# Performance work log

Measured on AMD Instinct MI355X. Metric: run time of the kernel, lower is better.

The kernel has to match this reference:

```python
import jax, jax.numpy as jnp
import numpy as np

VOCAB = 100000; D = 300; F_NUM = 768
M = 64; N = 16
SURF_L = 4; CTX_L = 50; DOC_L = 100; BODY_L = 200
HEADS = 5


def _conv_relu_avg(x, W, b):
    # x: [B, L, D] tokens-embedded; conv1d (valid) + relu + global avgpool -> [B, F]
    y = jax.lax.conv_general_dilated(x.transpose(0, 2, 1), W, (1,), 'VALID',
                                     dimension_numbers=('NCH', 'OIH', 'NCH'))
    return jax.nn.relu(y + b[None, :, None]).mean(axis=2)


def _mha(q, k, v, num_heads=HEADS):
    # split-head scaled dot-product attention (no learned projections), q:[Lq,D] k,v:[Lk,D]
    Lq, Dm = q.shape
    hd = Dm // num_heads
    qh = q.reshape(Lq, num_heads, hd).transpose(1, 0, 2)
    kh = k.reshape(k.shape[0], num_heads, hd).transpose(1, 0, 2)
    vh = v.reshape(v.shape[0], num_heads, hd).transpose(1, 0, 2)
    att = jax.nn.softmax(jnp.einsum('hqd,hkd->hqk', qh, kh) * (1.0 / np.sqrt(hd)), axis=-1)
    out = jnp.einsum('hqk,hkd->hqd', att, vh)
    return out.transpose(1, 0, 2).reshape(Lq, Dm)


def _cos(a, b, eps=1e-6):
    na = jnp.maximum(jnp.sqrt((a * a).sum(-1)), eps)
    nb = jnp.maximum(jnp.sqrt((b * b).sum(-1)), eps)
    return (a * b).sum(-1) / (na * nb)


def setup_inputs() -> dict:
    key = jax.random.key(0)
    ks = jax.random.split(key, 20)
    inp = {}
    inp['mention_entity'] = jnp.ones((M, N), dtype=jnp.int32)
    inp['m'] = M
    inp['n'] = N
    inp['mention_vec'] = jax.random.randint(ks[0], (M, SURF_L), 0, VOCAB)
    inp['context_vec'] = jax.random.randint(ks[1], (M, CTX_L), 0, VOCAB)
    inp['doc_vec'] = jax.random.randint(ks[2], (DOC_L,), 0, VOCAB)
    inp['title_vec'] = jax.random.normal(ks[3], (N, F_NUM), dtype=jnp.float32)
    inp['body_vec'] = jax.random.randint(ks[4], (N, BODY_L), 0, VOCAB)
    inp['sfeats'] = jnp.zeros((N, 1), dtype=jnp.float32)
    inp['m2c_prior'] = jax.random.uniform(ks[5], (N,), dtype=jnp.float32)
    inp['men2cands'] = jax.random.randint(ks[6], (M, N), 0, VOCAB)
    inp['contexts_ids'] = jax.random.randint(ks[7], (M, CTX_L), 0, VOCAB)
    inp['hand_features'] = jax.random.uniform(ks[8], (N, 1), dtype=jnp.float32)
    inp['bert_doc_vec'] = jax.random.normal(ks[9], (1, F_NUM), dtype=jnp.float32)
    # learned parameters
    inp['embed_table'] = jax.random.normal(ks[10], (VOCAB, D), dtype=jnp.float32) * 0.1
    inp['conv_ms_w'] = jax.random.normal(ks[11], (F_NUM, D, 2), dtype=jnp.float32) * 0.05
    inp['conv_ms_b'] = jnp.zeros((F_NUM,), dtype=jnp.float32)
    inp['conv_mc_w'] = jax.random.normal(ks[12], (F_NUM, D, 5), dtype=jnp.float32) * 0.05
    inp['conv_mc_b'] = jnp.zeros((F_NUM,), dtype=jnp.float32)
    inp['layer_local_w'] = jax.random.normal(ks[13], (7,), dtype=jnp.float32) * 0.3
    inp['layer_local_b'] = jnp.zeros((), dtype=jnp.float32)
    inp['att_w1'] = jax.random.normal(ks[14], (600, 300), dtype=jnp.float32) * 0.05
    inp['att_b1'] = jnp.zeros((300,), dtype=jnp.float32)
    inp['att_w2'] = jax.random.normal(ks[15], (300, 1), dtype=jnp.float32) * 0.05
    inp['att_b2'] = jnp.zeros((), dtype=jnp.float32)
    return inp


def reference(mention_entity, m, n, mention_vec, context_vec, doc_vec, title_vec,
              body_vec, sfeats, m2c_prior, men2cands, contexts_ids, hand_features,
              bert_doc_vec, embed_table, conv_ms_w, conv_ms_b, conv_mc_w, conv_mc_b,
              layer_local_w, layer_local_b, att_w1, att_b1, att_w2, att_b2):
    # per-mention conv features (vectorized over all mentions at once)
    ms = _conv_relu_avg(embed_table[mention_vec], conv_ms_w, conv_ms_b)   # [M,768]
    mc = _conv_relu_avg(embed_table[context_vec], conv_mc_w, conv_mc_b)   # [M,768]
    md = bert_doc_vec[0]                                                  # [768]
    doc_emb = embed_table[doc_vec]                                        # [100,300]
    body_emb = embed_table[body_vec]                                      # [N,200,300]

    # per-candidate cross attention doc<->body, max-pooled over query positions
    att_d_b = jax.vmap(lambda b: _mha(doc_emb, b, b).max(axis=0))(body_emb)          # [N,300]
    att_b_d = jax.vmap(lambda b: _mha(b, doc_emb, doc_emb).max(axis=0))(body_emb)    # [N,300]
    comb = jnp.concatenate([att_d_b, att_b_d], axis=-1)                              # [N,600]
    att_score = jax.nn.sigmoid(jax.nn.relu(comb @ att_w1 + att_b1) @ att_w2 + att_b2)[:, 0]  # [N]

    # LocalCtxAttRanker: candidate-vs-context attention score
    ctx_emb = embed_table[contexts_ids]                                   # [M,50,300]
    cand_emb = embed_table[men2cands]                                     # [M,N,300]
    tok = jnp.einsum('mnd,mtd->mnt', cand_emb, ctx_emb)                   # [M,N,50]
    p = jax.nn.softmax(tok.max(axis=1), axis=-1)                          # [M,50]
    ctxv = jnp.einsum('mt,mtd->md', p, ctx_emb)                           # [M,300]
    local_att = jnp.einsum('mnd,md->mn', cand_emb, ctxv)                  # [M,N]

    cos_st = _cos(ms[:, None, :], title_vec[None, :, :])                  # [M,N]
    cos_dt = _cos(md[None, :], title_vec)                                 # [N]
    cos_ct = _cos(mc[:, None, :], title_vec[None, :, :])                  # [M,N]

    Mm = ms.shape[0]
    bc = lambda v: jnp.broadcast_to(v[None, :], (Mm, v.shape[0]))
    # feature order matches torch.cat((hand_fea, prior, localAtt, attScore, C_score))
    feats = jnp.stack([bc(hand_features[:, 0]), bc(m2c_prior), local_att,
                       bc(att_score), cos_st, bc(cos_dt), cos_ct], axis=-1)  # [M,N,7]
    score = feats @ layer_local_w + layer_local_b                         # [M,N]

    # per-mention standardization (unbiased std, as torch.std), softmax and uniform renorm
    mu = score.mean(axis=1, keepdims=True)
    sd = score.std(axis=1, keepdims=True, ddof=1)
    z = (score - mu) / sd
    sm = jax.nn.softmax(z, axis=1)
    zmin = z.min(axis=1, keepdims=True)
    zmax = z.max(axis=1, keepdims=True)
    u = (z + 1.0 - zmin) / (zmax - zmin)
    u = u / u.sum(axis=1, keepdims=True)
    return (z, sm, u)
```

## Files before the change

### kernel.cpp

```cpp
#include <hip/hip_runtime.h>

#define MM 64
#define NN 16
#define DDIM 300
#define FNUM 768
#define SURF_LL 4
#define CTX_LL 50
#define DOC_LL 100
#define BODY_LL 200
#define NHEADS 5
#define HDIM 60

#define GM 2944
#define GK 1536
#define GN 768

typedef unsigned short u16;
typedef unsigned int u32;
typedef __attribute__((ext_vector_type(8))) short short8;
typedef __attribute__((ext_vector_type(4))) float f32x4;

#define OFF_MSG    0
#define OFF_CTX2G  76800
#define OFF_CANDG  1036800
#define OFF_MS     1344000
#define OFF_MC     1393152
#define OFF_PV0    1442304
#define OFF_PV1    1451904
#define OFF_ASC    1471104
#define OFF_LATT   1471120
#define OFF_ABF    1472144
#define OFF_WTMC   (OFF_ABF + GM*GK/2)
#define OFF_WTMS   (OFF_WTMC + GN*GK/2)
#define OFF_P      (OFF_WTMS + 600*768)

__device__ __forceinline__ u16 f2bf(float x) {
  union { float f; u32 u; } v; v.f = x;
  u32 r = v.u + 0x7FFFu + ((v.u >> 16) & 1u);
  return (u16)(r >> 16);
}

__global__ __launch_bounds__(256) void mega_prep_kernel(
    const float* __restrict__ embed,
    const int* __restrict__ mention_vec,
    const int* __restrict__ context_vec,
    const int* __restrict__ contexts_ids,
    const int* __restrict__ men2cands,
    const float* __restrict__ Wmc,
    const float* __restrict__ Wms,
    float* __restrict__ dst, float* __restrict__ mc,
    u32* __restrict__ Abf, u32* __restrict__ WTmc, float* __restrict__ WTms) {
  int bid = blockIdx.x;
  if (bid < 5250) {
    int e = bid * 256 + threadIdx.x;
    int row = e / DDIM;
    int col = e - row * DDIM;
    int tok;
    if (row < 256)       tok = mention_vec[row];
    else if (row < 3456) tok = contexts_ids[row - 256];
    else                 tok = men2cands[row - 3456];
    dst[e] = embed[(size_t)tok * DDIM + col];
  } else if (bid < 5442) {
    mc[(bid - 5250) * 256 + threadIdx.x] = 0.f;
  } else if (bid < 14274) {
    int idx = (bid - 5442) * 256 + threadIdx.x;
    int r = idx / (GK / 2);
    int kp = idx - r * (GK / 2);
    int k = kp * 2;
    int m = r / 46, t = r - m * 46;
    u32 out = 0;
#pragma unroll
    for (int j = 0; j < 2; j++) {
      int kj = k + j;
      u16 h = 0;
      if (kj < 1500) {
        int tap = kj / 300;
        int d = kj - tap * 300;
        int tok = context_vec[m * CTX_LL + t + tap];
        h = f2bf(embed[(size_t)tok * DDIM + d]);
      }
      out |= (u32)h << (16 * j);
    }
    Abf[idx] = out;
  } else if (bid < 16578) {
    int idx = (bid - 14274) * 256 + threadIdx.x;
    int n = idx / (GK / 2);
    int kp = idx - n * (GK / 2);
    int k = kp * 2;
    u32 out = 0;
#pragma unroll
    for (int j = 0; j < 2; j++) {
      int kj = k + j;
      u16 h = 0;
      if (kj < 1500) {
        int tap = kj / 300;
        int d = kj - tap * 300;
        h = f2bf(Wmc[(size_t)n * 1500 + d * 5 + tap]);
      }
      out |= (u32)h << (16 * j);
    }
    WTmc[idx] = out;
  } else {
    int idx = (bid - 16578) * 256 + threadIdx.x;
    int k = idx / FNUM;
    int f = idx - k * FNUM;
    WTms[idx] = Wms[(size_t)f * 600 + k];
  }
}

__global__ __launch_bounds__(256) void conv_gemm_kernel(
    const u16* __restrict__ A,
    const u16* __restrict__ B,
    const float* __restrict__ bias,
    float* __restrict__ mc) {
  int bn = blockIdx.x, bm = blockIdx.y;
  __shared__ u16 As[64][72];
  __shared__ u16 Bs[64][72];
  int tid = threadIdx.x;
  int w = tid >> 6, lane = tid & 63;
  int wr = w >> 1, wc = w & 1;
  int lg = lane >> 4, lm = lane & 15;
  f32x4 acc[2][2];
#pragma unroll
  for (int i = 0; i < 2; i++)
#pragma unroll
    for (int j = 0; j < 2; j++) acc[i][j] = (f32x4)0.f;
  int c0row = tid >> 3, ck = (tid & 7) * 8;
  const u16* Ag = A + (size_t)(bm * 64) * GK;
  const u16* Bg = B + (size_t)(bn * 64) * GK;
  for (int kt = 0; kt < GK / 64; kt++) {
    int k0 = kt * 64;
    uint4 av0 = *(const uint4*)(Ag + (size_t)c0row * GK + k0 + ck);
    uint4 av1 = *(const uint4*)(Ag + (size_t)(c0row + 32) * GK + k0 + ck);
    uint4 bv0 = *(const uint4*)(Bg + (size_t)c0row * GK + k0 + ck);
    uint4 bv1 = *(const uint4*)(Bg + (size_t)(c0row + 32) * GK + k0 + ck);
    __syncthreads();
    *(uint4*)&As[c0row][ck] = av0;
    *(uint4*)&As[c0row + 32][ck] = av1;
    *(uint4*)&Bs[c0row][ck] = bv0;
    *(uint4*)&Bs[c0row + 32][ck] = bv1;
    __syncthreads();
#pragma unroll
    for (int kk = 0; kk < 2; kk++) {
      short8 af0 = *(const short8*)&As[wr * 32 + lm][kk * 32 + lg * 8];
      short8 af1 = *(const short8*)&As[wr * 32 + 16 + lm][kk * 32 + lg * 8];
      short8 bf0 = *(const short8*)&Bs[wc * 32 + lm][kk * 32 + lg * 8];
      short8 bf1 = *(const short8*)&Bs[wc * 32 + 16 + lm][kk * 32 + lg * 8];
      acc[0][0] = __builtin_amdgcn_mfma_f32_16x16x32_bf16(af0, bf0, acc[0][0], 0, 0, 0);
      acc[0][1] = __builtin_amdgcn_mfma_f32_16x16x32_bf16(af0, bf1, acc[0][1], 0, 0, 0);
      acc[1][0] = __builtin_amdgcn_mfma_f32_16x16x32_bf16(af1, bf0, acc[1][0], 0, 0, 0);
      acc[1][1] = __builtin_amdgcn_mfma_f32_16x16x32_bf16(af1, bf1, acc[1][1], 0, 0, 0);
    }
  }
#pragma unroll
  for (int mf = 0; mf < 2; mf++)
#pragma unroll
    for (int nf = 0; nf < 2; nf++) {
      int col = bn * 64 + wc * 32 + nf * 16 + lm;
      float bb = bias[col];
      int base = bm * 64 + wr * 32 + mf * 16 + lg * 4;
      int mcur = base / 46;
      float s = 0.f;
#pragma unroll
      for (int r = 0; r < 4; r++) {
        float v = fmaxf(acc[mf][nf][r] + bb, 0.f) * (1.0f / 46.0f);
        int mm = (base + r) / 46;
        if (mm != mcur) { atomicAdd(&mc[mcur * FNUM + col], s); s = 0.f; mcur = mm; }
        s += v;
      }
      atomicAdd(&mc[mcur * FNUM + col], s);
    }
}

__device__ __forceinline__ void conv_ms_body(
    const float* __restrict__ msg, const float* __restrict__ WT,
    const float* __restrict__ B, float* __restrict__ ms, int b) {
  int m = b / 3, fi = b - m * 3;
  int f = fi * 256 + threadIdx.x;
  const float* x = msg + m * SURF_LL * DDIM;
  float a0 = 0.f, a1 = 0.f, a2 = 0.f;
  for (int d = 0; d < DDIM; d++) {
    float v0 = x[d], v1 = x[DDIM + d], v2 = x[2 * DDIM + d], v3 = x[3 * DDIM + d];
    float wA = WT[(size_t)(2 * d) * FNUM + f];
    float wB = WT[(size_t)(2 * d + 1) * FNUM + f];
    a0 += v0 * wA + v1 * wB;
    a1 += v1 * wA + v2 * wB;
    a2 += v2 * wA + v3 * wB;
  }
  float bb = B[f];
  float r = fmaxf(a0 + bb, 0.f) + fmaxf(a1 + bb, 0.f) + fmaxf(a2 + bb, 0.f);
  ms[m * FNUM + f] = r * (1.0f / 3.0f);
}

template <int DIR>
__device__ __forceinline__ void scores_body(
    const float* __restrict__ embed, const int* __restrict__ doc_vec,
    const int* __restrict__ body_vec, float* __restrict__ P, int b,
    float* __restrict__ smem) {
  constexpr int Lq = DIR ? 200 : 100;
  constexpr int Lk = DIR ? 100 : 200;
  constexpr int KPL = DIR ? 2 : 4;
  int qt = b / 80;
  int rem = b - qt * 80;
  int n = rem / 5, h = rem - n * 5;
  const int* qids = DIR ? body_vec + n * BODY_LL : doc_vec;
  const int* kids = DIR ? doc_vec : body_vec + n * BODY_LL;
  float* Ks = smem;
  float* Qs = smem + Lk * 62;
  for (int idx = threadIdx.x; idx < Lk * 15; idx += 256) {
    int r = idx / 15, c = idx - r * 15;
    float4 v = *(const float4*)(embed + (size_t)kids[r] * DDIM + h * HDIM + c * 4);
    float* dp = Ks + r * 62 + c * 4;
    dp[0] = v.x; dp[1] = v.y; dp[2] = v.z; dp[3] = v.w;
  }
  for (int idx = threadIdx.x; idx < 32 * 15; idx += 256) {
    int r = idx / 15, c = idx - r * 15;
    int q = qt * 32 + r; if (q >= Lq) q = Lq - 1;
    float4 v = *(const float4*)(embed + (size_t)qids[q] * DDIM + h * HDIM + c * 4);
    float* dp = Qs + r * 64 + c * 4;
    dp[0] = v.x; dp[1] = v.y; dp[2] = v.z; dp[3] = v.w;
  }
  __syncthreads();
  int w = threadIdx.x >> 6, lane = threadIdx.x & 63;
  int kcl[KPL];
#pragma unroll
  for (int j = 0; j < KPL; j++) {
    int kk = lane + 64 * j; kcl[j] = (kk < Lk) ? kk : (Lk - 1);
  }
  float acc[8][KPL];
#pragma unroll
  for (int i = 0; i < 8; i++)
#pragma unroll
    for (int j = 0; j < KPL; j++) acc[i][j] = 0.f;
  for (int d = 0; d < HDIM; d += 4) {
    float2 kva[KPL], kvb[KPL];
#pragma unroll
    for (int j = 0; j < KPL; j++) {
      kva[j] = *(const float2*)&Ks[kcl[j] * 62 + d];
      kvb[j] = *(const float2*)&Ks[kcl[j] * 62 + d + 2];
    }
#pragma unroll
    for (int i = 0; i < 8; i++) {
      float4 qv = *(const float4*)&Qs[(w * 8 + i) * 64 + d];
#pragma unroll
      for (int j = 0; j < KPL; j++)
        acc[i][j] += qv.x * kva[j].x + qv.y * kva[j].y +
                     qv.z * kvb[j].x + qv.w * kvb[j].y;
    }
  }
  const float scale = 0.12909944487358056f;
#pragma unroll
  for (int i = 0; i < 8; i++) {
    int q = qt * 32 + w * 8 + i;
    float mx = -1e30f;
#pragma unroll
    for (int j = 0; j < KPL; j++)
      if (lane + 64 * j < Lk) mx = fmaxf(mx, acc[i][j]);
#pragma unroll
    for (int o = 32; o >= 1; o >>= 1) mx = fmaxf(mx, __shfl_xor(mx, o));
    float mxs = mx * scale;
    float p[KPL];
    float s = 0.f;
#pragma unroll
    for (int j = 0; j < KPL; j++) {
      p[j] = (lane + 64 * j < Lk) ? __expf(acc[i][j] * scale - mxs) : 0.f;
      s += p[j];
    }
#pragma unroll
    for (int o = 32; o >= 1; o >>= 1) s += __shfl_xor(s, o);
    float inv = 1.0f / s;
    if (q < Lq) {
      float* rowp = P + (size_t)((n * 2 + DIR) * NHEADS + h) * 20000 + q * Lk;
#pragma unroll
      for (int j = 0; j < KPL; j++) {
        int kk = lane + 64 * j;
        if (kk < Lk) rowp[kk] = p[j] * inv;
      }
    }
  }
}

__device__ __forceinline__ void tokctxv_body(
    const float* __restrict__ candg, const float* __restrict__ ctx2g,
    float* __restrict__ local_att, int m, float* __restrict__ smem) {
  float* cand  = smem;
  float* ctx   = smem + 4800;
  float* tokb  = smem + 9600;
  float* tkmx  = smem + 9872;
  float* pp    = smem + 9936;
  float* sctxv = smem + 10000;
  int tid = threadIdx.x;
  for (int i = tid; i < NN * DDIM; i += 256)
    cand[i] = candg[(size_t)m * NN * DDIM + i];
  int nI = tid >> 4, tt = tid & 15;
  for (int tile = 0; tile < 4; tile++) {
    int cbase = tile * 16;
    __syncthreads();
    for (int i = tid; i < 16 * DDIM; i += 256) {
      int rr = i / DDIM, cc = i - rr * DDIM;
      int t = cbase + rr;
      ctx[rr * DDIM + cc] = (t < CTX_LL) ? ctx2g[(size_t)(m * CTX_LL + t) * DDIM + cc] : 0.f;
    }
    __syncthreads();
    const float4* ca = (const float4*)(cand + nI * DDIM);
    const float4* cb = (const float4*)(ctx + tt * DDIM);
    float dsum = 0.f;
#pragma unroll
    for (int c = 0; c < 75; c++) {
      float4 a = ca[c], b = cb[c];
      dsum += a.x * b.x + a.y * b.y + a.z * b.z + a.w * b.w;
    }
    tokb[nI * 17 + tt] = dsum;
    __syncthreads();
    if (tid < 16) {
      float mx = -1e30f;
      for (int nn = 0; nn < NN; nn++) mx = fmaxf(mx, tokb[nn * 17 + tid]);
      int t = cbase + tid;
      if (t < CTX_LL) tkmx[t] = mx;
    }
  }
  __syncthreads();
  if (tid < 64) {
    float v = (tid < CTX_LL) ? tkmx[tid] : -1e30f;
    float mx = v;
#pragma unroll
    for (int o = 32; o >= 1; o >>= 1) mx = fmaxf(mx, __shfl_xor(mx, o));
    float e = (tid < CTX_LL) ? expf(v - mx) : 0.f;
    float s = e;
#pragma unroll
    for (int o = 32; o >= 1; o >>= 1) s += __shfl_xor(s, o);
    pp[tid] = e / s;
  }
  __syncthreads();
  for (int d = tid; d < DDIM; d += 256) {
    float acc = 0.f;
    for (int t = 0; t < CTX_LL; t++)
      acc += pp[t] * ctx2g[(size_t)(m * CTX_LL + t) * DDIM + d];
    sctxv[d] = acc;
  }
  __syncthreads();
  int j = tid & 15;
  float dd = 0.f;
  for (int i = j; i < DDIM; i += 16) dd += cand[nI * DDIM + i] * sctxv[i];
#pragma unroll
  for (int o = 8; o >= 1; o >>= 1) dd += __shfl_xor(dd, o);
  if (j == 0) local_att[m * NN + nI] = dd;
}

__global__ __launch_bounds__(256) void mega_mid_kernel(
    const float* __restrict__ embed,
    const int* __restrict__ doc_vec,
    const int* __restrict__ body_vec,
    const float* __restrict__ msg,
    const float* __restrict__ WTms,
    const float* __restrict__ Bms,
    const float* __restrict__ candg,
    const float* __restrict__ ctx2g,
    float* __restrict__ ms,
    float* __restrict__ P,
    float* __restrict__ local_att) {
  __shared__ float smem[14448];
  int bid = blockIdx.x;
  if (bid < 192) {
    conv_ms_body(msg, WTms, Bms, ms, bid);
  } else if (bid < 512) {
    scores_body<0>(embed, doc_vec, body_vec, P, bid - 192, smem);
  } else if (bid < 1072) {
    scores_body<1>(embed, doc_vec, body_vec, P, bid - 512, smem);
  } else {
    tokctxv_body(candg, ctx2g, local_att, bid - 1072, smem);
  }
}

__global__ __launch_bounds__(256) void attn_pv_kernel(
    const float* __restrict__ embed,
    const int* __restrict__ doc_vec,
    const int* __restrict__ body_vec,
    const float* __restrict__ P,
    float* __restrict__ pv0,
    float* __restrict__ pv1) {
  int bid = blockIdx.x;
  int dir, pt, n, h;
  if (bid < 160) { dir = 0; h = bid % 5; n = (bid / 5) % 16; pt = bid / 80; }
  else { int b = bid - 160; dir = 1; h = b % 5; n = (b / 5) % 16; pt = b / 80; }
  int Lq = dir ? 200 : 100;
  int Lk = dir ? 100 : 200;
  int Lk4 = Lk >> 2;
  int K4STR = dir ? 27 : 51;
  const int* kids = dir ? doc_vec : body_vec + n * BODY_LL;
  __shared__ float4 Kt4[60 * 51];
  __shared__ float red[4][64];
  float* Ktf = (float*)Kt4;
  int RS = K4STR * 4;
  for (int idx = threadIdx.x; idx < Lk * 15; idx += 256) {
    int r = idx / 15, c = idx - r * 15;
    float4 v = *(const float4*)(embed + (size_t)kids[r] * DDIM + h * HDIM + c * 4);
    Ktf[(c * 4 + 0) * RS + r] = v.x;
    Ktf[(c * 4 + 1) * RS + r] = v.y;
    Ktf[(c * 4 + 2) * RS + r] = v.z;
    Ktf[(c * 4 + 3) * RS + r] = v.w;
  }
  __syncthreads();
  int lane = threadIdx.x & 63;
  int w = __builtin_amdgcn_readfirstlane(threadIdx.x >> 6);
  int dl = (lane < HDIM) ? lane : (HDIM - 1);
  const float4* Krow = Kt4 + dl * K4STR;
  const float* Pb = P + (size_t)((n * 2 + dir) * NHEADS + h) * 20000;
  float omax = -1e30f;
#pragma unroll
  for (int p = 0; p < 4; p++) {
    int q0 = pt * 64 + p * 16 + w * 4;
    int qa0 = min(q0, Lq - 1), qa1 = min(q0 + 1, Lq - 1);
    int qa2 = min(q0 + 2, Lq - 1), qa3 = min(q0 + 3, Lq - 1);
    const float4* P0 = (const float4*)(Pb + (size_t)qa0 * Lk);
    const float4* P1 = (const float4*)(Pb + (size_t)qa1 * Lk);
    const float4* P2 = (const float4*)(Pb + (size_t)qa2 * Lk);
    const float4* P3 = (const float4*)(Pb + (size_t)qa3 * Lk);
    float o0 = 0.f, o1 = 0.f, o2 = 0.f, o3 = 0.f;
    for (int k4 = 0; k4 < Lk4; k4++) {
      float4 pp0 = P0[k4], pp1 = P1[k4], pp2 = P2[k4], pp3 = P3[k4];
      float4 kk = Krow[k4];
      o0 += pp0.x * kk.x + pp0.y * kk.y + pp0.z * kk.z + pp0.w * kk.w;
      o1 += pp1.x * kk.x + pp1.y * kk.y + pp1.z * kk.z + pp1.w * kk.w;
      o2 += pp2.x * kk.x + pp2.y * kk.y + pp2.z * kk.z + pp2.w * kk.w;
      o3 += pp3.x * kk.x + pp3.y * kk.y + pp3.z * kk.z + pp3.w * kk.w;
    }
    if (q0 < Lq)     omax = fmaxf(omax, o0);
    if (q0 + 1 < Lq) omax = fmaxf(omax, o1);
    if (q0 + 2 < Lq) omax = fmaxf(omax, o2);
    if (q0 + 3 < Lq) omax = fmaxf(omax, o3);
  }
  red[threadIdx.x >> 6][lane] = omax;
  __syncthreads();
  if (threadIdx.x < 64 && lane < HDIM) {
    float m4 = fmaxf(fmaxf(red[0][lane], red[1][lane]),
                     fmaxf(red[2][lane], red[3][lane]));
    float* dst = dir ? pv1 + (size_t)((n * NHEADS + h) * 4 + pt) * HDIM
                     : pv0 + (size_t)((n * NHEADS + h) * 2 + pt) * HDIM;
    dst[lane] = m4;
  }
}

__global__ __launch_bounds__(256) void mlp_kernel(
    const float* __restrict__ pv0, const float* __restrict__ pv1,
    const float* __restrict__ w1, const float* __restrict__ b1,
    const float* __restrict__ w2, const float* __restrict__ b2,
    float* __restrict__ att_score) {
  int n = blockIdx.x, tid = threadIdx.x;
  __shared__ float comb[600];
  for (int idx = tid; idx < 300; idx += 256) {
    int h = idx / 60, d = idx - h * 60;
    float mx = -1e30f;
#pragma unroll
    for (int pt = 0; pt < 2; pt++)
      mx = fmaxf(mx, pv0[(size_t)((n * NHEADS + h) * 2 + pt) * HDIM + d]);
    comb[idx] = mx;
    mx = -1e30f;
#pragma unroll
    for (int pt = 0; pt < 4; pt++)
      mx = fmaxf(mx, pv1[(size_t)((n * NHEADS + h) * 4 + pt) * HDIM + d]);
    comb[300 + idx] = mx;
  }
  __syncthreads();
  float partial = 0.f;
  for (int j = tid; j < 300; j += 256) {
    float hh = b1[j];
    for (int k = 0; k < 600; k++) hh += comb[k] * w1[k * 300 + j];
    partial += fmaxf(hh, 0.f) * w2[j];
  }
  __shared__ float redd[256];
  redd[tid] = partial;
  __syncthreads();
  for (int s = 128; s > 0; s >>= 1) {
    if (tid < s) redd[tid] += redd[tid + s];
    __syncthreads();
  }
  if (tid == 0) att_score[n] = 1.0f / (1.0f + expf(-(redd[0] + b2[0])));
}

__global__ __launch_bounds__(256) void final_kernel(
    const float* __restrict__ ms,
    const float* __restrict__ mc,
    const float* __restrict__ title,
    const float* __restrict__ bert,
    const float* __restrict__ att_score,
    const float* __restrict__ m2c_prior,
    const float* __restrict__ hand,
    const float* __restrict__ local_att,
    const float* __restrict__ w7,
    const float* __restrict__ b7,
    float* __restrict__ out) {
  int m = blockIdx.x, tid = threadIdx.x;
  __shared__ float sms[FNUM], smc[FNUM], smd[FNUM];
  __shared__ float snorm[3], sscore[16], wred[3][4];
  for (int i = tid; i < FNUM; i += 256) {
    sms[i] = ms[m * FNUM + i];
    smc[i] = mc[m * FNUM + i];
    smd[i] = bert[i];
  }
  __syncthreads();
  float p1 = 0.f, p2 = 0.f, p3 = 0.f;
  for (int i = tid; i < FNUM; i += 256) {
    float a = sms[i], b = smc[i], c = smd[i];
    p1 += a * a; p2 += b * b; p3 += c * c;
  }
#pragma unroll
  for (int o = 32; o >= 1; o >>= 1) {
    p1 += __shfl_xor(p1, o); p2 += __shfl_xor(p2, o); p3 += __shfl_xor(p3, o);
  }
  int wid = tid >> 6, lane = tid & 63;
  if (lane == 0) { wred[0][wid] = p1; wred[1][wid] = p2; wred[2][wid] = p3; }
  __syncthreads();
  if (tid == 0) {
    snorm[0] = fmaxf(sqrtf(wred[0][0] + wred[0][1] + wred[0][2] + wred[0][3]), 1e-6f);
    snorm[1] = fmaxf(sqrtf(wred[1][0] + wred[1][1] + wred[1][2] + wred[1][3]), 1e-6f);
    snorm[2] = fmaxf(sqrtf(wred[2][0] + wred[2][1] + wred[2][2] + wred[2][3]), 1e-6f);
  }
  __syncthreads();
  int nI = tid >> 4, j = tid & 15;
  float d1 = 0.f, d2 = 0.f, d3 = 0.f, d4 = 0.f;
  for (int i = j; i < FNUM; i += 16) {
    float t = title[nI * FNUM + i];
    d1 += sms[i] * t; d2 += smc[i] * t; d3 += smd[i] * t; d4 += t * t;
  }
#pragma unroll
  for (int o = 8; o >= 1; o >>= 1) {
    d1 += __shfl_xor(d1, o); d2 += __shfl_xor(d2, o);
    d3 += __shfl_xor(d3, o); d4 += __shfl_xor(d4, o);
  }
  if (j == 0) {
    float nt = fmaxf(sqrtf(d4), 1e-6f);
    float cos_st = d1 / (snorm[0] * nt);
    float cos_ct = d2 / (snorm[1] * nt);
    float cos_dt = d3 / (snorm[2] * nt);
    float score = hand[nI] * w7[0] + m2c_prior[nI] * w7[1] +
                  local_att[m * NN + nI] * w7[2] + att_score[nI] * w7[3] +
                  cos_st * w7[4] + cos_dt * w7[5] + cos_ct * w7[6] + b7[0];
    sscore[nI] = score;
  }
  __syncthreads();
  if (tid < 16) {
    float x = sscore[tid];
    float s = x;
#pragma unroll
    for (int o = 8; o >= 1; o >>= 1) s += __shfl_xor(s, o);
    float mu = s * (1.0f / 16.0f);
    float dv = (x - mu) * (x - mu);
    float vs = dv;
#pragma unroll
    for (int o = 8; o >= 1; o >>= 1) vs += __shfl_xor(vs, o);
    float sd = sqrtf(vs * (1.0f / 15.0f));
    float z = (x - mu) / sd;
    float zm = z;
#pragma unroll
    for (int o = 8; o >= 1; o >>= 1) zm = fmaxf(zm, __shfl_xor(zm, o));
    float e = expf(z - zm);
    float es = e;
#pragma unroll
    for (int o = 8; o >= 1; o >>= 1) es += __shfl_xor(es, o);
    float sm = e / es;
    float zmin = z;
#pragma unroll
    for (int o = 8; o >= 1; o >>= 1) zmin = fminf(zmin, __shfl_xor(zmin, o));
    float u0 = (z + 1.0f - zmin) / (zm - zmin);
    float us = u0;
#pragma unroll
    for (int o = 8; o >= 1; o >>= 1) us += __shfl_xor(us, o);
    float u = u0 / us;
    out[m * NN + tid] = z;
    out[MM * NN + m * NN + tid] = sm;
    out[2 * MM * NN + m * NN + tid] = u;
  }
}

extern "C" void kernel_launch(void* const* d_in, const int* in_sizes, int n_in,
                              void* d_out, int out_size, void* d_ws, size_t ws_size,
                              hipStream_t stream) {
  const int*   mention_vec   = (const int*)d_in[3];
  const int*   context_vec   = (const int*)d_in[4];
  const int*   doc_vec       = (const int*)d_in[5];
  const float* title_vec     = (const float*)d_in[6];
  const int*   body_vec      = (const int*)d_in[7];
  const float* m2c_prior     = (const float*)d_in[9];
  const int*   men2cands     = (const int*)d_in[10];
  const int*   contexts_ids  = (const int*)d_in[11];
  const float* hand_features = (const float*)d_in[12];
  const float* bert_doc_vec  = (const float*)d_in[13];
  const float* embed_table   = (const float*)d_in[14];
  const float* conv_ms_w     = (const float*)d_in[15];
  const float* conv_ms_b     = (const float*)d_in[16];
  const float* conv_mc_w     = (const float*)d_in[17];
  const float* conv_mc_b     = (const float*)d_in[18];
  const float* layer_local_w = (const float*)d_in[19];
  const float* layer_local_b = (const float*)d_in[20];
  const float* att_w1        = (const float*)d_in[21];
  const float* att_b1        = (const float*)d_in[22];
  const float* att_w2        = (const float*)d_in[23];
  const float* att_b2        = (const float*)d_in[24];

  float* ws     = (float*)d_ws;
  float* msg    = ws + OFF_MSG;
  float* ctx2g  = ws + OFF_CTX2G;
  float* candg  = ws + OFF_CANDG;
  float* ms     = ws + OFF_MS;
  float* mc     = ws + OFF_MC;
  float* pv0    = ws + OFF_PV0;
  float* pv1    = ws + OFF_PV1;
  float* att_sc = ws + OFF_ASC;
  float* latt   = ws + OFF_LATT;
  u16*   Abf    = (u16*)(ws + OFF_ABF);
  u16*   WTmc   = (u16*)(ws + OFF_WTMC);
  float* WTms   = ws + OFF_WTMS;
  float* P      = ws + OFF_P;
  float* out    = (float*)d_out;

  mega_prep_kernel<<<dim3(18378), dim3(256), 0, stream>>>(
      embed_table, mention_vec, context_vec, contexts_ids, men2cands,
      conv_mc_w, conv_ms_w, ws, mc, (u32*)Abf, (u32*)WTmc, WTms);
  conv_gemm_kernel<<<dim3(GN / 64, GM / 64), dim3(256), 0, stream>>>(
      Abf, WTmc, conv_mc_b, mc);
  mega_mid_kernel<<<dim3(1136), dim3(256), 0, stream>>>(
      embed_table, doc_vec, body_vec, msg, WTms, conv_ms_b, candg, ctx2g,
      ms, P, latt);
  attn_pv_kernel<<<dim3(480), dim3(256), 0, stream>>>(
      embed_table, doc_vec, body_vec, P, pv0, pv1);
  mlp_kernel<<<dim3(NN), dim3(256), 0, stream>>>(pv0, pv1, att_w1, att_b1, att_w2, att_b2, att_sc);
  final_kernel<<<dim3(MM), dim3(256), 0, stream>>>(
      ms, mc, title_vec, bert_doc_vec, att_sc, m2c_prior, hand_features,
      latt, layer_local_w, layer_local_b, out);
}
```

Baseline: 420.1 us.

## Fuse attention PV into scores kernel and split MLP across more blocks

The attention probability matrix P is no longer written to global memory. Each scores block now keeps its softmax rows in registers and shared memory, computes P·V against the keys already staged in shared memory, and writes per-tile max-pooled partials, so the separate attn_pv kernel and its P round trip disappear. The MLP moves from 16 blocks to 80, each handling a slice of hidden units, and combines results with atomicAdd into a logit buffer that the prep kernel zeroes. The final sigmoid moves into final_kernel. In exchange, shared memory use and register pressure in the mid kernel rise, and float atomics make the summation order nondeterministic.

Result: faster. 399.1 us (-5.0%).

```diff
diff --git a/kernel.cpp b/kernel.cpp
--- a/kernel.cpp
+++ b/kernel.cpp
@@ -26,13 +26,12 @@
 #define OFF_MS     1344000
 #define OFF_MC     1393152
 #define OFF_PV0    1442304
-#define OFF_PV1    1451904
-#define OFF_ASC    1471104
-#define OFF_LATT   1471120
-#define OFF_ABF    1472144
+#define OFF_PV1    1461504
+#define OFF_ASC    1495104
+#define OFF_LATT   1495120
+#define OFF_ABF    1496144
 #define OFF_WTMC   (OFF_ABF + GM*GK/2)
 #define OFF_WTMS   (OFF_WTMC + GN*GK/2)
-#define OFF_P      (OFF_WTMS + 600*768)
 
 __device__ __forceinline__ u16 f2bf(float x) {
   union { float f; u32 u; } v; v.f = x;
@@ -49,6 +48,7 @@
     const float* __restrict__ Wmc,
     const float* __restrict__ Wms,
     float* __restrict__ dst, float* __restrict__ mc,
+    float* __restrict__ att_logit,
     u32* __restrict__ Abf, u32* __restrict__ WTmc, float* __restrict__ WTms) {
   int bid = blockIdx.x;
   if (bid < 5250) {
@@ -62,8 +62,10 @@
     dst[e] = embed[(size_t)tok * DDIM + col];
   } else if (bid < 5442) {
     mc[(bid - 5250) * 256 + threadIdx.x] = 0.f;
-  } else if (bid < 14274) {
-    int idx = (bid - 5442) * 256 + threadIdx.x;
+  } else if (bid == 5442) {
+    if (threadIdx.x < NN) att_logit[threadIdx.x] = 0.f;
+  } else if (bid < 14275) {
+    int idx = (bid - 5443) * 256 + threadIdx.x;
     int r = idx / (GK / 2);
     int kp = idx - r * (GK / 2);
     int k = kp * 2;
@@ -82,8 +84,8 @@
       out |= (u32)h << (16 * j);
     }
     Abf[idx] = out;
-  } else if (bid < 16578) {
-    int idx = (bid - 14274) * 256 + threadIdx.x;
+  } else if (bid < 16579) {
+    int idx = (bid - 14275) * 256 + threadIdx.x;
     int n = idx / (GK / 2);
     int kp = idx - n * (GK / 2);
     int k = kp * 2;
@@ -101,7 +103,7 @@
     }
     WTmc[idx] = out;
   } else {
-    int idx = (bid - 16578) * 256 + threadIdx.x;
+    int idx = (bid - 16579) * 256 + threadIdx.x;
     int k = idx / FNUM;
     int f = idx - k * FNUM;
     WTms[idx] = Wms[(size_t)f * 600 + k];
@@ -193,20 +195,24 @@
 }
 
 template <int DIR>
-__device__ __forceinline__ void scores_body(
+__device__ __forceinline__ void scores_pv_body(
     const float* __restrict__ embed, const int* __restrict__ doc_vec,
-    const int* __restrict__ body_vec, float* __restrict__ P, int b,
+    const int* __restrict__ body_vec, float* __restrict__ pvp, int b,
     float* __restrict__ smem) {
   constexpr int Lq = DIR ? 200 : 100;
   constexpr int Lk = DIR ? 100 : 200;
   constexpr int KPL = DIR ? 2 : 4;
+  constexpr int NQT = DIR ? 7 : 4;
+  constexpr int NHALF = DIR ? 1 : 2;
   int qt = b / 80;
   int rem = b - qt * 80;
   int n = rem / 5, h = rem - n * 5;
   const int* qids = DIR ? body_vec + n * BODY_LL : doc_vec;
   const int* kids = DIR ? doc_vec : body_vec + n * BODY_LL;
   float* Ks = smem;
-  float* Qs = smem + Lk * 62;
+  float* Qs = smem + 12400;
+  float* Pl = smem + 12400;
+  float* red = smem + 15600;
   for (int idx = threadIdx.x; idx < Lk * 15; idx += 256) {
     int r = idx / 15, c = idx - r * 15;
     float4 v = *(const float4*)(embed + (size_t)kids[r] * DDIM + h * HDIM + c * 4);
@@ -251,7 +257,6 @@
   const float scale = 0.12909944487358056f;
 #pragma unroll
   for (int i = 0; i < 8; i++) {
-    int q = qt * 32 + w * 8 + i;
     float mx = -1e30f;
 #pragma unroll
     for (int j = 0; j < KPL; j++)
@@ -269,14 +274,52 @@
 #pragma unroll
     for (int o = 32; o >= 1; o >>= 1) s += __shfl_xor(s, o);
     float inv = 1.0f / s;
-    if (q < Lq) {
-      float* rowp = P + (size_t)((n * 2 + DIR) * NHEADS + h) * 20000 + q * Lk;
-#pragma unroll
-      for (int j = 0; j < KPL; j++) {
-        int kk = lane + 64 * j;
-        if (kk < Lk) rowp[kk] = p[j] * inv;
+#pragma unroll
+    for (int j = 0; j < KPL; j++) acc[i][j] = p[j] * inv;
+  }
+  __syncthreads();
+  float o[8];
+#pragma unroll
+  for (int i = 0; i < 8; i++) o[i] = 0.f;
+  int dl = (lane < HDIM) ? lane : (HDIM - 1);
+#pragma unroll
+  for (int half = 0; half < NHALF; half++) {
+    int kbase = half * 100;
+#pragma unroll
+    for (int j = 0; j < KPL; j++) {
+      int kk = lane + 64 * j;
+      int rel = kk - kbase;
+      if (rel >= 0 && rel < 100 && kk < Lk) {
+#pragma unroll
+        for (int i = 0; i < 8; i++)
+          Pl[(w * 8 + i) * 100 + rel] = acc[i][j];
       }
     }
+    for (int k4 = 0; k4 < 25; k4++) {
+      int k = kbase + k4 * 4;
+      float kv0 = Ks[(k + 0) * 62 + dl];
+      float kv1 = Ks[(k + 1) * 62 + dl];
+      float kv2 = Ks[(k + 2) * 62 + dl];
+      float kv3 = Ks[(k + 3) * 62 + dl];
+#pragma unroll
+      for (int i = 0; i < 8; i++) {
+        float4 pq = *(const float4*)&Pl[(w * 8 + i) * 100 + k4 * 4];
+        o[i] += pq.x * kv0 + pq.y * kv1 + pq.z * kv2 + pq.w * kv3;
+      }
+    }
+  }
+  float omax = -1e30f;
+#pragma unroll
+  for (int i = 0; i < 8; i++) {
+    int q = qt * 32 + w * 8 + i;
+    if (q < Lq) omax = fmaxf(omax, o[i]);
+  }
+  red[w * 64 + lane] = omax;
+  __syncthreads();
+  if (threadIdx.x < 64 && lane < HDIM) {
+    float m4 = fmaxf(fmaxf(red[0 * 64 + lane], red[1 * 64 + lane]),
+                     fmaxf(red[2 * 64 + lane], red[3 * 64 + lane]));
+    pvp[((size_t)(n * NHEADS + h) * NQT + qt) * HDIM + lane] = m4;
   }
 }
 
@@ -357,125 +400,66 @@
     const float* __restrict__ candg,
     const float* __restrict__ ctx2g,
     float* __restrict__ ms,
-    float* __restrict__ P,
+    float* __restrict__ pv0,
+    float* __restrict__ pv1,
     float* __restrict__ local_att) {
-  __shared__ float smem[14448];
+  __shared__ float smem[15856];
   int bid = blockIdx.x;
   if (bid < 192) {
     conv_ms_body(msg, WTms, Bms, ms, bid);
   } else if (bid < 512) {
-    scores_body<0>(embed, doc_vec, body_vec, P, bid - 192, smem);
+    scores_pv_body<0>(embed, doc_vec, body_vec, pv0, bid - 192, smem);
   } else if (bid < 1072) {
-    scores_body<1>(embed, doc_vec, body_vec, P, bid - 512, smem);
+    scores_pv_body<1>(embed, doc_vec, body_vec, pv1, bid - 512, smem);
   } else {
     tokctxv_body(candg, ctx2g, local_att, bid - 1072, smem);
-  }
-}
-
-__global__ __launch_bounds__(256) void attn_pv_kernel(
-    const float* __restrict__ embed,
-    const int* __restrict__ doc_vec,
-    const int* __restrict__ body_vec,
-    const float* __restrict__ P,
-    float* __restrict__ pv0,
-    float* __restrict__ pv1) {
-  int bid = blockIdx.x;
-  int dir, pt, n, h;
-  if (bid < 160) { dir = 0; h = bid % 5; n = (bid / 5) % 16; pt = bid / 80; }
-  else { int b = bid - 160; dir = 1; h = b % 5; n = (b / 5) % 16; pt = b / 80; }
-  int Lq = dir ? 200 : 100;
-  int Lk = dir ? 100 : 200;
-  int Lk4 = Lk >> 2;
-  int K4STR = dir ? 27 : 51;
-  const int* kids = dir ? doc_vec : body_vec + n * BODY_LL;
-  __shared__ float4 Kt4[60 * 51];
-  __shared__ float red[4][64];
-  float* Ktf = (float*)Kt4;
-  int RS = K4STR * 4;
-  for (int idx = threadIdx.x; idx < Lk * 15; idx += 256) {
-    int r = idx / 15, c = idx - r * 15;
-    float4 v = *(const float4*)(embed + (size_t)kids[r] * DDIM + h * HDIM + c * 4);
-    Ktf[(c * 4 + 0) * RS + r] = v.x;
-    Ktf[(c * 4 + 1) * RS + r] = v.y;
-    Ktf[(c * 4 + 2) * RS + r] = v.z;
-    Ktf[(c * 4 + 3) * RS + r] = v.w;
-  }
-  __syncthreads();
-  int lane = threadIdx.x & 63;
-  int w = __builtin_amdgcn_readfirstlane(threadIdx.x >> 6);
-  int dl = (lane < HDIM) ? lane : (HDIM - 1);
-  const float4* Krow = Kt4 + dl * K4STR;
-  const float* Pb = P + (size_t)((n * 2 + dir) * NHEADS + h) * 20000;
-  float omax = -1e30f;
-#pragma unroll
-  for (int p = 0; p < 4; p++) {
-    int q0 = pt * 64 + p * 16 + w * 4;
-    int qa0 = min(q0, Lq - 1), qa1 = min(q0 + 1, Lq - 1);
-    int qa2 = min(q0 + 2, Lq - 1), qa3 = min(q0 + 3, Lq - 1);
-    const float4* P0 = (const float4*)(Pb + (size_t)qa0 * Lk);
-    const float4* P1 = (const float4*)(Pb + (size_t)qa1 * Lk);
-    const float4* P2 = (const float4*)(Pb + (size_t)qa2 * Lk);
-    const float4* P3 = (const float4*)(Pb + (size_t)qa3 * Lk);
-    float o0 = 0.f, o1 = 0.f, o2 = 0.f, o3 = 0.f;
-    for (int k4 = 0; k4 < Lk4; k4++) {
-      float4 pp0 = P0[k4], pp1 = P1[k4], pp2 = P2[k4], pp3 = P3[k4];
-      float4 kk = Krow[k4];
-      o0 += pp0.x * kk.x + pp0.y * kk.y + pp0.z * kk.z + pp0.w * kk.w;
-      o1 += pp1.x * kk.x + pp1.y * kk.y + pp1.z * kk.z + pp1.w * kk.w;
-      o2 += pp2.x * kk.x + pp2.y * kk.y + pp2.z * kk.z + pp2.w * kk.w;
-      o3 += pp3.x * kk.x + pp3.y * kk.y + pp3.z * kk.z + pp3.w * kk.w;
-    }
-    if (q0 < Lq)     omax = fmaxf(omax, o0);
-    if (q0 + 1 < Lq) omax = fmaxf(omax, o1);
-    if (q0 + 2 < Lq) omax = fmaxf(omax, o2);
-    if (q0 + 3 < Lq) omax = fmaxf(omax, o3);
-  }
-  red[threadIdx.x >> 6][lane] = omax;
-  __syncthreads();
-  if (threadIdx.x < 64 && lane < HDIM) {
-    float m4 = fmaxf(fmaxf(red[0][lane], red[1][lane]),
-                     fmaxf(red[2][lane], red[3][lane]));
-    float* dst = dir ? pv1 + (size_t)((n * NHEADS + h) * 4 + pt) * HDIM
-                     : pv0 + (size_t)((n * NHEADS + h) * 2 + pt) * HDIM;
-    dst[lane] = m4;
   }
 }
 
 __global__ __launch_bounds__(256) void mlp_kernel(
     const float* __restrict__ pv0, const float* __restrict__ pv1,
     const float* __restrict__ w1, const float* __restrict__ b1,
-    const float* __restrict__ w2, const float* __restrict__ b2,
-    float* __restrict__ att_score) {
-  int n = blockIdx.x, tid = threadIdx.x;
+    const float* __restrict__ w2,
+    float* __restrict__ att_logit) {
+  int bid = blockIdx.x;
+  int n = bid / 5, jc = bid - n * 5;
+  int tid = threadIdx.x;
   __shared__ float comb[600];
-  for (int idx = tid; idx < 300; idx += 256) {
-    int h = idx / 60, d = idx - h * 60;
+  __shared__ float partial[4][64];
+  for (int idx = tid; idx < 600; idx += 256) {
+    int side = idx >= 300;
+    int pos = idx - side * 300;
+    int h = pos / 60, d = pos - h * 60;
     float mx = -1e30f;
-#pragma unroll
-    for (int pt = 0; pt < 2; pt++)
-      mx = fmaxf(mx, pv0[(size_t)((n * NHEADS + h) * 2 + pt) * HDIM + d]);
+    if (!side) {
+#pragma unroll
+      for (int pt = 0; pt < 4; pt++)
+        mx = fmaxf(mx, pv0[(size_t)((n * NHEADS + h) * 4 + pt) * HDIM + d]);
+    } else {
+#pragma unroll
+      for (int pt = 0; pt < 7; pt++)
+        mx = fmaxf(mx, pv1[(size_t)((n * NHEADS + h) * 7 + pt) * HDIM + d]);
+    }
     comb[idx] = mx;
-    mx = -1e30f;
-#pragma unroll
-    for (int pt = 0; pt < 4; pt++)
-      mx = fmaxf(mx, pv1[(size_t)((n * NHEADS + h) * 4 + pt) * HDIM + d]);
-    comb[300 + idx] = mx;
-  }
-  __syncthreads();
-  float partial = 0.f;
-  for (int j = tid; j < 300; j += 256) {
-    float hh = b1[j];
-    for (int k = 0; k < 600; k++) hh += comb[k] * w1[k * 300 + j];
-    partial += fmaxf(hh, 0.f) * w2[j];
-  }
-  __shared__ float redd[256];
-  redd[tid] = partial;
-  __syncthreads();
-  for (int s = 128; s > 0; s >>= 1) {
-    if (tid < s) redd[tid] += redd[tid + s];
-    __syncthreads();
-  }
-  if (tid == 0) att_score[n] = 1.0f / (1.0f + expf(-(redd[0] + b2[0])));
+  }
+  __syncthreads();
+  int w = tid >> 6, lane = tid & 63;
+  int jl = (lane < 60) ? lane : 59;
+  int jg = jc * 60 + jl;
+  float acc = 0.f;
+  for (int k = w; k < 600; k += 4)
+    acc += comb[k] * w1[(size_t)k * 300 + jg];
+  partial[w][lane] = acc;
+  __syncthreads();
+  if (tid < 64) {
+    float hv = partial[0][lane] + partial[1][lane] +
+               partial[2][lane] + partial[3][lane];
+    float hj = fmaxf(hv + b1[jg], 0.f) * w2[jg];
+    if (lane >= 60) hj = 0.f;
+#pragma unroll
+    for (int o = 32; o >= 1; o >>= 1) hj += __shfl_xor(hj, o);
+    if (lane == 0) atomicAdd(&att_logit[n], hj);
+  }
 }
 
 __global__ __launch_bounds__(256) void final_kernel(
@@ -483,7 +467,8 @@
     const float* __restrict__ mc,
     const float* __restrict__ title,
     const float* __restrict__ bert,
-    const float* __restrict__ att_score,
+    const float* __restrict__ att_logit,
+    const float* __restrict__ b2,
     const float* __restrict__ m2c_prior,
     const float* __restrict__ hand,
     const float* __restrict__ local_att,
@@ -533,8 +518,9 @@
     float cos_st = d1 / (snorm[0] * nt);
     float cos_ct = d2 / (snorm[1] * nt);
     float cos_dt = d3 / (snorm[2] * nt);
+    float asc = 1.0f / (1.0f + expf(-(att_logit[nI] + b2[0])));
     float score = hand[nI] * w7[0] + m2c_prior[nI] * w7[1] +
-                  local_att[m * NN + nI] * w7[2] + att_score[nI] * w7[3] +
+                  local_att[m * NN + nI] * w7[2] + asc * w7[3] +
                   cos_st * w7[4] + cos_dt * w7[5] + cos_ct * w7[6] + b7[0];
     sscore[nI] = score;
   }
@@ -606,26 +592,24 @@
   float* mc     = ws + OFF_MC;
   float* pv0    = ws + OFF_PV0;
   float* pv1    = ws + OFF_PV1;
-  float* att_sc = ws + OFF_ASC;
+  float* att_lg = ws + OFF_ASC;
   float* latt   = ws + OFF_LATT;
   u16*   Abf    = (u16*)(ws + OFF_ABF);
   u16*   WTmc   = (u16*)(ws + OFF_WTMC);
   float* WTms   = ws + OFF_WTMS;
-  float* P      = ws + OFF_P;
   float* out    = (float*)d_out;
 
-  mega_prep_kernel<<<dim3(18378), dim3(256), 0, stream>>>(
+  mega_prep_kernel<<<dim3(18379), dim3(256), 0, stream>>>(
       embed_table, mention_vec, context_vec, contexts_ids, men2cands,
-      conv_mc_w, conv_ms_w, ws, mc, (u32*)Abf, (u32*)WTmc, WTms);
+      conv_mc_w, conv_ms_w, ws, mc, att_lg, (u32*)Abf, (u32*)WTmc, WTms);
   conv_gemm_kernel<<<dim3(GN / 64, GM / 64), dim3(256), 0, stream>>>(
       Abf, WTmc, conv_mc_b, mc);
   mega_mid_kernel<<<dim3(1136), dim3(256), 0, stream>>>(
       embed_table, doc_vec, body_vec, msg, WTms, conv_ms_b, candg, ctx2g,
-      ms, P, latt);
-  attn_pv_kernel<<<dim3(480), dim3(256), 0, stream>>>(
-      embed_table, doc_vec, body_vec, P, pv0, pv1);
-  mlp_kernel<<<dim3(NN), dim3(256), 0, stream>>>(pv0, pv1, att_w1, att_b1, att_w2, att_b2, att_sc);
+      ms, pv0, pv1, latt);
+  mlp_kernel<<<dim3(80), dim3(256), 0, stream>>>(
+      pv0, pv1, att_w1, att_b1, att_w2, att_lg);
   final_kernel<<<dim3(MM), dim3(256), 0, stream>>>(
-      ms, mc, title_vec, bert_doc_vec, att_sc, m2c_prior, hand_features,
-      latt, layer_local_w, layer_local_b, out);
-}
+      ms, mc, title_vec, bert_doc_vec, att_lg, att_b2, m2c_prior,
+      hand_features, latt, layer_local_w, layer_local_b, out);
+}
```
